# Performance work log

Measured on AMD Instinct MI355X. Metric: run time of the kernel, lower is better.

## Reference

```python
import jax, jax.numpy as jnp
import numpy as np

# dims: L=seq_len, B=batch, D=n_d (hidden), PROJ=n_proj, H=heads, DEPTH=layers, V=vocab
L, B, D, PROJ, H, DEPTH, V = 1024, 4, 1024, 256, 8, 4, 32000
HD = PROJ // H          # head dim = 32
NEG = -10000.0          # additive causal mask value used by Model.set_mask


def setup_inputs() -> dict:
    key = jax.random.key(0)
    ks = jax.random.split(key, 12)
    s = (3.0 / D) ** 0.5  # init used by Model.init_weights (layer_norm-style)
    return {
        "x": jax.random.randint(ks[0], (L, B), 0, V),
        "y": jax.random.randint(ks[1], (L, B), 0, V),
        "hidden": jnp.zeros((DEPTH, B, D), jnp.float32),            # init_hidden
        "emb_W": jax.random.uniform(ks[2], (V, D), jnp.float32, -s, s),
        # SRU++ attention transform per layer: q-proj, kv-proj, output to 3*D (U matrices)
        "W1": jax.random.normal(ks[3], (DEPTH, D, PROJ), jnp.float32) / np.float32(np.sqrt(D)),
        "W2": jax.random.normal(ks[4], (DEPTH, PROJ, 2 * PROJ), jnp.float32) / np.float32(np.sqrt(PROJ)),
        "W3": jax.random.normal(ks[5], (DEPTH, PROJ, 3 * D), jnp.float32) / np.float32(np.sqrt(PROJ)),
        "alpha": jax.random.normal(ks[6], (DEPTH,), jnp.float32) * 0.1,  # rezero scalar (nonzero so attn path is live)
        "weight_c": jax.random.normal(ks[7], (DEPTH, 2 * D), jnp.float32) * 0.1,  # (v_f, v_r)
        # bias = (b_f, b_r); forget bias initialized to highway_bias = -3
        "bias": jnp.concatenate([jnp.full((DEPTH, D), -3.0, jnp.float32), jnp.zeros((DEPTH, D), jnp.float32)], axis=-1),
        "Wout": jax.random.uniform(ks[8], (D, V), jnp.float32, -s, s),
        "bout": jnp.zeros((V,), jnp.float32),
    }


def _attention_transform(h, W1, W2, W3, alpha, mask):
    # SRUppAttention (no memory, no layer_norm, dropout=0)
    z = jnp.einsum('lbd,dp->lbp', h, W1)                 # (L,B,PROJ) query / residual
    kv = jnp.einsum('lbp,pq->lbq', z, W2)                # (L,B,2*PROJ)
    k, v = jnp.split(kv, 2, axis=-1)
    q = z.reshape(L, B, H, HD) * (HD ** -0.5)
    k = k.reshape(L, B, H, HD)
    v = v.reshape(L, B, H, HD)
    scores = jnp.einsum('lbhd,sbhd->bhls', q, k) + mask  # causal additive mask
    attn = jax.nn.softmax(scores, axis=-1)
    out = jnp.einsum('bhls,sbhd->lbhd', attn, v).reshape(L, B, PROJ)
    out = out * alpha + z                                # rezero residual
    return jnp.einsum('lbp,pk->lbk', out, W3)            # U: (L,B,3*D)


def _sru_recurrence(U, residual, c0, vf, vr, bf, br):
    # SRU elementwise highway recurrence (k=3, identity activation, no rescale)
    u = U.reshape(L, B, D, 3)
    u0 = u[..., 0]
    u1 = u[..., 1] + bf
    u2 = u[..., 2] + br

    def step(c, xs):
        u0t, u1t, u2t, rt = xs                           # each (B,D)
        f = jax.nn.sigmoid(u1t + vf * c)
        c = f * c + (1.0 - f) * u0t
        r = jax.nn.sigmoid(u2t + vr * c)
        h = r * c + (1.0 - r) * rt                       # highway on layer input
        return c, h

    c_last, hs = jax.lax.scan(step, c0, (u0, u1, u2, residual))
    return hs, c_last


def reference(x, y, hidden, emb_W, W1, W2, W3, alpha, weight_c, bias, Wout, bout):
    mask = jnp.triu(jnp.full((L, L), NEG, jnp.float32), 1)   # Model.set_mask, mem_len=0
    h = emb_W[x]                                             # (L,B,D) embedding lookup
    for i in range(DEPTH):
        U = _attention_transform(h, W1[i], W2[i], W3[i], alpha[i], mask)
        h, _ = _sru_recurrence(U, h, hidden[i],
                               weight_c[i, :D], weight_c[i, D:],
                               bias[i, :D], bias[i, D:])
    logits = jnp.einsum('lbd,dv->lbv', h, Wout) + bout       # (L,B,V)
    logp = jax.nn.log_softmax(logits, axis=-1)
    loss = -jnp.take_along_axis(logp, y[..., None], axis=-1)[..., 0]  # (L,B) per-token CE
    return loss
```

## Files before the change

### kernel.cpp

```cpp
#include <hip/hip_runtime.h>
#include <hip/hip_bf16.h>
#include <stdint.h>

#define L_ 1024
#define B_ 4
#define D_ 1024
#define PROJ_ 256
#define H_ 8
#define V_ 32000
#define M_ 4096

typedef __bf16 bf16x8 __attribute__((ext_vector_type(8)));
typedef float f32x4 __attribute__((ext_vector_type(4)));

#define AS3(p) ((__attribute__((address_space(3))) void*)(p))
#define AS1(p) ((const __attribute__((address_space(1))) void*)(p))

__global__ __launch_bounds__(256) void k_embed(const int* __restrict__ x,
                                               const float* __restrict__ emb,
                                               __hip_bfloat16* __restrict__ h) {
  int gid = blockIdx.x * 256 + threadIdx.x;
  int row = gid >> 8;
  int d0 = (gid & 255) << 2;
  int tok = x[row];
  const float4 v = *(const float4*)(emb + (size_t)tok * D_ + d0);
  union { __hip_bfloat16 o[4]; uint2 u; } cv;
  cv.o[0] = __float2bfloat16(v.x);
  cv.o[1] = __float2bfloat16(v.y);
  cv.o[2] = __float2bfloat16(v.z);
  cv.o[3] = __float2bfloat16(v.w);
  *(uint2*)(h + (size_t)row * D_ + d0) = cv.u;
}

__global__ __launch_bounds__(256) void k_transpose(const float* __restrict__ in,
                                                   __hip_bfloat16* __restrict__ out,
                                                   int K, int N,
                                                   long in_stride, long out_stride) {
  __shared__ float t[64][65];
  in += (size_t)blockIdx.z * in_stride;
  out += (size_t)blockIdx.z * out_stride;
  int n0 = blockIdx.x * 64, k0 = blockIdx.y * 64;
  int r = threadIdx.x >> 4, c4 = (threadIdx.x & 15) << 2;
#pragma unroll
  for (int p = 0; p < 4; p++) {
    float4 v = *(const float4*)(in + (size_t)(k0 + p * 16 + r) * N + n0 + c4);
    t[p * 16 + r][c4 + 0] = v.x;
    t[p * 16 + r][c4 + 1] = v.y;
    t[p * 16 + r][c4 + 2] = v.z;
    t[p * 16 + r][c4 + 3] = v.w;
  }
  __syncthreads();
  int n = threadIdx.x >> 2, kg = (threadIdx.x & 3) << 4;
  union { __hip_bfloat16 b[16]; uint4 u[2]; } cv;
#pragma unroll
  for (int i = 0; i < 16; i++) cv.b[i] = __float2bfloat16(t[kg + i][n]);
  uint4* op = (uint4*)(out + (size_t)(n0 + n) * K + k0 + kg);
  op[0] = cv.u[0];
  op[1] = cv.u[1];
}

template <bool CLS>
__global__ __launch_bounds__(256) void k_gemm_bt(
    const __hip_bfloat16* __restrict__ A, const __hip_bfloat16* __restrict__ Bt,
    __hip_bfloat16* __restrict__ C, int K, int N,
    const float* __restrict__ bout, const int* __restrict__ y,
    float2* __restrict__ lse, float* __restrict__ logitY) {
  __shared__ __hip_bfloat16 As[128 * 64];
  __shared__ __hip_bfloat16 Bs[128 * 64];
  const int tid = threadIdx.x;
  const int lane = tid & 63, wave = tid >> 6;
  const int quad = lane >> 4, l16 = lane & 15;
  const int wm = wave & 1, wn = wave >> 1;
  const int row0 = blockIdx.x * 128, col0 = blockIdx.y * 128;

  f32x4 acc[4][4] = {};

  const __hip_bfloat16* Abase = A + (size_t)row0 * K;
  const __hip_bfloat16* Bbase = Bt + (size_t)col0 * K;
  const int m_s = tid >> 3;
  const int ko_sw = (((tid & 7) ^ (m_s & 7)) << 3);
  const int xr = l16 & 7;

  for (int k0 = 0; k0 < K; k0 += 64) {
    __syncthreads();
#pragma unroll
    for (int call = 0; call < 4; call++) {
      int m = m_s + call * 32;
      __builtin_amdgcn_global_load_lds(AS1(Abase + (size_t)m * K + k0 + ko_sw),
                                       AS3(As + (call * 256 + wave * 64) * 8),
                                       16, 0, 0);
      __builtin_amdgcn_global_load_lds(AS1(Bbase + (size_t)m * K + k0 + ko_sw),
                                       AS3(Bs + (call * 256 + wave * 64) * 8),
                                       16, 0, 0);
    }
    __syncthreads();
#pragma unroll
    for (int kk = 0; kk < 2; kk++) {
      bf16x8 af[4], bfr[4];
#pragma unroll
      for (int mi = 0; mi < 4; mi++)
        af[mi] = *(const bf16x8*)(As + (wm * 64 + mi * 16 + l16) * 64 +
                                  (((kk * 4 + quad) ^ xr) << 3));
#pragma unroll
      for (int ni = 0; ni < 4; ni++)
        bfr[ni] = *(const bf16x8*)(Bs + (wn * 64 + ni * 16 + l16) * 64 +
                                   (((kk * 4 + quad) ^ xr) << 3));
#pragma unroll
      for (int mi = 0; mi < 4; mi++)
#pragma unroll
        for (int ni = 0; ni < 4; ni++)
          acc[mi][ni] = __builtin_amdgcn_mfma_f32_16x16x32_bf16(af[mi], bfr[ni],
                                                                acc[mi][ni], 0, 0, 0);
    }
  }

  if constexpr (!CLS) {
#pragma unroll
    for (int mi = 0; mi < 4; mi++)
#pragma unroll
      for (int ni = 0; ni < 4; ni++)
#pragma unroll
        for (int r = 0; r < 4; r++) {
          int row = row0 + wm * 64 + mi * 16 + quad * 4 + r;
          int col = col0 + wn * 64 + ni * 16 + l16;
          C[(size_t)row * N + col] = __float2bfloat16(acc[mi][ni][r]);
        }
  } else {
    const int chunk = blockIdx.y * 2 + wn;
    float bv[4];
#pragma unroll
    for (int ni = 0; ni < 4; ni++)
      bv[ni] = bout[col0 + wn * 64 + ni * 16 + l16];
#pragma unroll
    for (int mi = 0; mi < 4; mi++) {
#pragma unroll
      for (int r = 0; r < 4; r++) {
        int row = row0 + wm * 64 + mi * 16 + quad * 4 + r;
        float v0 = acc[mi][0][r] + bv[0];
        float v1 = acc[mi][1][r] + bv[1];
        float v2 = acc[mi][2][r] + bv[2];
        float v3 = acc[mi][3][r] + bv[3];
        int yv = y[row];
        int cb = col0 + wn * 64 + l16;
        if (yv == cb + 0)  logitY[row] = v0;
        if (yv == cb + 16) logitY[row] = v1;
        if (yv == cb + 32) logitY[row] = v2;
        if (yv == cb + 48) logitY[row] = v3;
        float m = fmaxf(fmaxf(v0, v1), fmaxf(v2, v3));
#pragma unroll
        for (int off = 1; off < 16; off <<= 1)
          m = fmaxf(m, __shfl_xor(m, off, 64));
        float s = __expf(v0 - m) + __expf(v1 - m) + __expf(v2 - m) + __expf(v3 - m);
#pragma unroll
        for (int off = 1; off < 16; off <<= 1)
          s += __shfl_xor(s, off, 64);
        if (l16 == 0)
          lse[(size_t)chunk * M_ + row] = make_float2(m, s);
      }
    }
  }
}

__global__ __launch_bounds__(512, 2) void k_gemm_cls256(
    const __hip_bfloat16* __restrict__ A, const __hip_bfloat16* __restrict__ Bt,
    int K, const float* __restrict__ bout, const int* __restrict__ y,
    float2* __restrict__ lse, float* __restrict__ logitY) {
  __shared__ __align__(16) __hip_bfloat16 As[2][16384];
  __shared__ __align__(16) __hip_bfloat16 Bs[2][16384];
  const int tid = threadIdx.x;
  const int lane = tid & 63, wave = tid >> 6;
  const int quad = lane >> 4, l16 = lane & 15;
  const int wm = wave >> 2, wn = wave & 3;

  const int bid = blockIdx.y * 16 + blockIdx.x;
  const int swzb = (bid & 7) * 250 + (bid >> 3);
  const int bx = swzb & 15, by = swzb >> 4;
  const int row0 = bx * 256, col0 = by * 256;

  const int m_l = wave * 8 + (lane >> 3);
  const int sw = ((lane & 7) ^ (lane >> 3)) << 3;
  const __hip_bfloat16* Ag = A + (size_t)(row0 + m_l) * K + sw;
  const __hip_bfloat16* Bg = Bt + (size_t)(col0 + m_l) * K + sw;

#define STAGE_A(buf, r, ko)                                                   \
  __builtin_amdgcn_global_load_lds(AS1(Ag + (size_t)(r) * 64 * K + (ko)),     \
                                   AS3(&As[buf][((r) * 64 + wave * 8) * 64]), \
                                   16, 0, 0)
#define STAGE_B(buf, r, ko)                                                   \
  __builtin_amdgcn_global_load_lds(AS1(Bg + (size_t)(r) * 64 * K + (ko)),     \
                                   AS3(&Bs[buf][((r) * 64 + wave * 8) * 64]), \
                                   16, 0, 0)

  const int aoff = (wm * 128 + l16) * 64;
  const int boff = (wn * 64 + l16) * 64;
  const int cc0 = ((quad) ^ (l16 & 7)) << 3;
  const int cc1 = ((4 + quad) ^ (l16 & 7)) << 3;

  f32x4 acc[8][4] = {};
  bf16x8 a4[4], b4[4];

#define PH_PRE(buf, cck, mlo, READB)                                          \
  do {                                                                        \
    if (READB) {                                                              \
      _Pragma("unroll") for (int ni = 0; ni < 4; ++ni)                        \
          b4[ni] = *(const bf16x8*)(&Bs[buf][boff + ni * 1024 + (cck)]);      \
    }                                                                         \
    _Pragma("unroll") for (int mi = 0; mi < 4; ++mi)                          \
        a4[mi] = *(const bf16x8*)(&As[buf][aoff + ((mlo) + mi) * 1024 + (cck)]); \
  } while (0)

#define PH_MFMA(mlo)                                                          \
  do {                                                                        \
    __builtin_amdgcn_s_barrier();                                             \
    asm volatile("s_waitcnt lgkmcnt(0)" ::: "memory");                        \
    __builtin_amdgcn_sched_barrier(0);                                        \
    __builtin_amdgcn_s_setprio(1);                                            \
    _Pragma("unroll") for (int mi = 0; mi < 4; ++mi)                          \
        _Pragma("unroll") for (int ni = 0; ni < 4; ++ni)                      \
            acc[(mlo) + mi][ni] = __builtin_amdgcn_mfma_f32_16x16x32_bf16(    \
                a4[mi], b4[ni], acc[(mlo) + mi][ni], 0, 0, 0);                \
    __builtin_amdgcn_s_setprio(0);                                            \
  } while (0)

#define BAR() __builtin_amdgcn_s_barrier()

  STAGE_A(0, 0, 0); STAGE_A(0, 1, 0); STAGE_A(0, 2, 0); STAGE_A(0, 3, 0);
  STAGE_B(0, 0, 0); STAGE_B(0, 1, 0); STAGE_B(0, 2, 0); STAGE_B(0, 3, 0);
  STAGE_B(1, 0, 64); STAGE_B(1, 1, 64); STAGE_B(1, 2, 64); STAGE_B(1, 3, 64);
  STAGE_A(1, 0, 64); STAGE_A(1, 2, 64);
  asm volatile("s_waitcnt vmcnt(6)" ::: "memory");
  BAR();

  for (int i = 0; i < 7; ++i) {
    const size_t kT1 = (size_t)i * 128 + 64;
    const size_t kS0 = (size_t)i * 128 + 128;
    const size_t kS1 = (size_t)i * 128 + 192;
    PH_PRE(0, cc0, 0, 1);
    STAGE_A(1, 1, kT1); STAGE_A(1, 3, kT1);
    PH_MFMA(0); BAR();
    PH_PRE(0, cc0, 4, 0);
    PH_MFMA(4); BAR();
    PH_PRE(0, cc1, 0, 1);
    PH_MFMA(0); BAR();
    PH_PRE(0, cc1, 4, 0);
    STAGE_B(0, 0, kS0); STAGE_B(0, 1, kS0);
    PH_MFMA(4);
    asm volatile("s_waitcnt vmcnt(2)" ::: "memory");
    BAR();
    PH_PRE(1, cc0, 0, 1);
    STAGE_B(0, 2, kS0); STAGE_B(0, 3, kS0);
    PH_MFMA(0); BAR();
    PH_PRE(1, cc0, 4, 0);
    STAGE_A(0, 0, kS0); STAGE_A(0, 2, kS0);
    PH_MFMA(4); BAR();
    PH_PRE(1, cc1, 0, 1);
    STAGE_A(0, 1, kS0); STAGE_A(0, 3, kS0);
    PH_MFMA(0); BAR();
    PH_PRE(1, cc1, 4, 0);
    STAGE_B(1, 0, kS1); STAGE_B(1, 1, kS1); STAGE_B(1, 2, kS1); STAGE_B(1, 3, kS1);
    STAGE_A(1, 0, kS1); STAGE_A(1, 2, kS1);
    PH_MFMA(4);
    asm volatile("s_waitcnt vmcnt(6)" ::: "memory");
    BAR();
  }
  {
    const size_t kT1 = (size_t)7 * 128 + 64;
    PH_PRE(0, cc0, 0, 1);
    STAGE_A(1, 1, kT1); STAGE_A(1, 3, kT1);
    PH_MFMA(0); BAR();
    PH_PRE(0, cc0, 4, 0);
    PH_MFMA(4); BAR();
    PH_PRE(0, cc1, 0, 1);
    PH_MFMA(0); BAR();
    PH_PRE(0, cc1, 4, 0);
    PH_MFMA(4);
    asm volatile("s_waitcnt vmcnt(0)" ::: "memory");
    BAR();
    PH_PRE(1, cc0, 0, 1);
    PH_MFMA(0); BAR();
    PH_PRE(1, cc0, 4, 0);
    PH_MFMA(4); BAR();
    PH_PRE(1, cc1, 0, 1);
    PH_MFMA(0); BAR();
    PH_PRE(1, cc1, 4, 0);
    PH_MFMA(4);
  }

  const int chunk = by * 4 + wn;
  float bv[4];
#pragma unroll
  for (int ni = 0; ni < 4; ++ni)
    bv[ni] = bout[col0 + wn * 64 + ni * 16 + l16];
#pragma unroll
  for (int mi = 0; mi < 8; ++mi) {
#pragma unroll
    for (int r = 0; r < 4; ++r) {
      int row = row0 + wm * 128 + mi * 16 + quad * 4 + r;
      float v0 = acc[mi][0][r] + bv[0];
      float v1 = acc[mi][1][r] + bv[1];
      float v2 = acc[mi][2][r] + bv[2];
      float v3 = acc[mi][3][r] + bv[3];
      int yv = y[row];
      int cb = col0 + wn * 64 + l16;
      if (yv == cb + 0)  logitY[row] = v0;
      if (yv == cb + 16) logitY[row] = v1;
      if (yv == cb + 32) logitY[row] = v2;
      if (yv == cb + 48) logitY[row] = v3;
      float m = fmaxf(fmaxf(v0, v1), fmaxf(v2, v3));
#pragma unroll
      for (int off = 1; off < 16; off <<= 1)
        m = fmaxf(m, __shfl_xor(m, off, 64));
      float s = __expf(v0 - m) + __expf(v1 - m) + __expf(v2 - m) + __expf(v3 - m);
#pragma unroll
      for (int off = 1; off < 16; off <<= 1)
        s += __shfl_xor(s, off, 64);
      if (l16 == 0)
        lse[(size_t)chunk * M_ + row] = make_float2(m, s);
    }
  }
#undef STAGE_A
#undef STAGE_B
#undef PH_PRE
#undef PH_MFMA
#undef BAR
}

__global__ __launch_bounds__(256) void k_gemm_cls_f32(
    const __hip_bfloat16* __restrict__ A, const float* __restrict__ B,
    int K, int N, const float* __restrict__ bout, const int* __restrict__ y,
    float2* __restrict__ lse, float* __restrict__ logitY) {
  __shared__ __hip_bfloat16 As[128 * 40];
  __shared__ __hip_bfloat16 Bs[128 * 40];
  const int tid = threadIdx.x;
  const int lane = tid & 63, wave = tid >> 6;
  const int quad = lane >> 4, l16 = lane & 15;
  const int wm = wave & 1, wn = wave >> 1;
  const int row0 = blockIdx.x * 128, col0 = blockIdx.y * 128;
  f32x4 acc[4][4] = {};
  const int a_m = tid >> 1, a_k = (tid & 1) << 4;
  const int b_k = tid >> 3, b_n = (tid & 7) << 4;
  for (int k0 = 0; k0 < K; k0 += 32) {
    const uint4* ap = (const uint4*)(A + (size_t)(row0 + a_m) * K + k0 + a_k);
    uint4 av0 = ap[0];
    uint4 av1 = ap[1];
    const float* bp = B + (size_t)(k0 + b_k) * N + col0 + b_n;
    float4 bv0 = *(const float4*)(bp + 0);
    float4 bv1 = *(const float4*)(bp + 4);
    float4 bv2 = *(const float4*)(bp + 8);
    float4 bv3 = *(const float4*)(bp + 12);
    __syncthreads();
    *(uint4*)(As + a_m * 40 + a_k) = av0;
    *(uint4*)(As + a_m * 40 + a_k + 8) = av1;
    {
      float tmp[16] = {bv0.x, bv0.y, bv0.z, bv0.w, bv1.x, bv1.y, bv1.z, bv1.w,
                       bv2.x, bv2.y, bv2.z, bv2.w, bv3.x, bv3.y, bv3.z, bv3.w};
#pragma unroll
      for (int j = 0; j < 16; j++)
        Bs[(b_n + j) * 40 + b_k] = __float2bfloat16(tmp[j]);
    }
    __syncthreads();
    bf16x8 af[4], bfr[4];
#pragma unroll
    for (int mi = 0; mi < 4; mi++)
      af[mi] = *(const bf16x8*)(As + (wm * 64 + mi * 16 + l16) * 40 + quad * 8);
#pragma unroll
    for (int ni = 0; ni < 4; ni++)
      bfr[ni] = *(const bf16x8*)(Bs + (wn * 64 + ni * 16 + l16) * 40 + quad * 8);
#pragma unroll
    for (int mi = 0; mi < 4; mi++)
#pragma unroll
      for (int ni = 0; ni < 4; ni++)
        acc[mi][ni] = __builtin_amdgcn_mfma_f32_16x16x32_bf16(af[mi], bfr[ni],
                                                              acc[mi][ni], 0, 0, 0);
  }
  const int chunk = blockIdx.y * 2 + wn;
  float bv[4];
#pragma unroll
  for (int ni = 0; ni < 4; ni++)
    bv[ni] = bout[col0 + wn * 64 + ni * 16 + l16];
#pragma unroll
  for (int mi = 0; mi < 4; mi++) {
#pragma unroll
    for (int r = 0; r < 4; r++) {
      int row = row0 + wm * 64 + mi * 16 + quad * 4 + r;
      float v0 = acc[mi][0][r] + bv[0];
      float v1 = acc[mi][1][r] + bv[1];
      float v2 = acc[mi][2][r] + bv[2];
      float v3 = acc[mi][3][r] + bv[3];
      int yv = y[row];
      int cb = col0 + wn * 64 + l16;
      if (yv == cb + 0)  logitY[row] = v0;
      if (yv == cb + 16) logitY[row] = v1;
      if (yv == cb + 32) logitY[row] = v2;
      if (yv == cb + 48) logitY[row] = v3;
      float m = fmaxf(fmaxf(v0, v1), fmaxf(v2, v3));
#pragma unroll
      for (int off = 1; off < 16; off <<= 1)
        m = fmaxf(m, __shfl_xor(m, off, 64));
      float s = __expf(v0 - m) + __expf(v1 - m) + __expf(v2 - m) + __expf(v3 - m);
#pragma unroll
      for (int off = 1; off < 16; off <<= 1)
        s += __shfl_xor(s, off, 64);
      if (l16 == 0)
        lse[(size_t)chunk * M_ + row] = make_float2(m, s);
    }
  }
}

__global__ __launch_bounds__(256) void k_attn_mfma(
    const __hip_bfloat16* __restrict__ z, const __hip_bfloat16* __restrict__ kv,
    __hip_bfloat16* __restrict__ ao, const float* __restrict__ alpha_p) {
  __shared__ __hip_bfloat16 Qs[64 * 40];
  __shared__ __hip_bfloat16 Ks[128 * 40];
  __shared__ __hip_bfloat16 Vt[32 * 136];
  __shared__ __hip_bfloat16 Ps[64 * 136];
  const int tid = threadIdx.x;
  const int lane = tid & 63, wave = tid >> 6;
  const int quad = lane >> 4, l16 = lane & 15;
  const int bh = blockIdx.y, b = bh >> 3, h = bh & 7;
  const int q0 = blockIdx.x * 64;
  const float scale = 0.17677669529663687f;

  {
    int r = tid >> 2, c = (tid & 3) << 3;
    *(uint4*)(Qs + r * 40 + c) =
        *(const uint4*)(z + ((size_t)(q0 + r) * B_ + b) * PROJ_ + h * 32 + c);
  }

  float m_i[4] = {-1e30f, -1e30f, -1e30f, -1e30f};
  float l_i[4] = {0.f, 0.f, 0.f, 0.f};
  f32x4 o_acc[2] = {};

  const int ntile = (q0 + 191) >> 7;

  for (int t = 0; t < ntile; t++) {
    const int s0 = t << 7;
    __syncthreads();
    {
      int r = tid >> 1, c = (tid & 1) << 4;
      const uint4* kp =
          (const uint4*)(kv + ((size_t)(s0 + r) * B_ + b) * 512 + h * 32 + c);
      *(uint4*)(Ks + r * 40 + c) = kp[0];
      *(uint4*)(Ks + r * 40 + c + 8) = kp[1];
    }
    {
      int s = tid >> 1, dbase = (tid & 1) << 4;
      const __hip_bfloat16* vp =
          kv + ((size_t)(s0 + s) * B_ + b) * 512 + 256 + h * 32 + dbase;
      union { uint4 u; __hip_bfloat16 e[8]; } t0, t1;
      t0.u = *(const uint4*)vp;
      t1.u = *(const uint4*)(vp + 8);
#pragma unroll
      for (int j = 0; j < 8; j++) {
        Vt[(dbase + j) * 136 + s] = t0.e[j];
        Vt[(dbase + 8 + j) * 136 + s] = t1.e[j];
      }
    }
    __syncthreads();

    f32x4 sacc[8] = {};
    {
      bf16x8 aq = *(const bf16x8*)(Qs + (wave * 16 + l16) * 40 + quad * 8);
#pragma unroll
      for (int ni = 0; ni < 8; ni++) {
        bf16x8 bk = *(const bf16x8*)(Ks + (ni * 16 + l16) * 40 + quad * 8);
        sacc[ni] = __builtin_amdgcn_mfma_f32_16x16x32_bf16(aq, bk, sacc[ni], 0, 0, 0);
      }
    }

#pragma unroll
    for (int r = 0; r < 4; r++) {
      const int qrow = q0 + wave * 16 + quad * 4 + r;
      float mx = -1e30f;
#pragma unroll
      for (int ni = 0; ni < 8; ni++) {
        int s = s0 + ni * 16 + l16;
        float v = (s <= qrow) ? sacc[ni][r] * scale : -1e30f;
        sacc[ni][r] = v;
        mx = fmaxf(mx, v);
      }
#pragma unroll
      for (int off = 1; off < 16; off <<= 1)
        mx = fmaxf(mx, __shfl_xor(mx, off, 64));
      float mnew = fmaxf(m_i[r], mx);
      float al = __expf(m_i[r] - mnew);
      m_i[r] = mnew;
      float ps = 0.f;
#pragma unroll
      for (int ni = 0; ni < 8; ni++) {
        float p = __expf(sacc[ni][r] - mnew);
        Ps[(wave * 16 + quad * 4 + r) * 136 + ni * 16 + l16] = __float2bfloat16(p);
        ps += p;
      }
#pragma unroll
      for (int off = 1; off < 16; off <<= 1)
        ps += __shfl_xor(ps, off, 64);
      l_i[r] = l_i[r] * al + ps;
      o_acc[0][r] *= al;
      o_acc[1][r] *= al;
    }

#pragma unroll
    for (int ks = 0; ks < 4; ks++) {
      bf16x8 ap = *(const bf16x8*)(Ps + (wave * 16 + l16) * 136 + ks * 32 + quad * 8);
#pragma unroll
      for (int ni = 0; ni < 2; ni++) {
        bf16x8 bv = *(const bf16x8*)(Vt + (ni * 16 + l16) * 136 + ks * 32 + quad * 8);
        o_acc[ni] = __builtin_amdgcn_mfma_f32_16x16x32_bf16(ap, bv, o_acc[ni], 0, 0, 0);
      }
    }
  }

  const float arz = alpha_p[0];
#pragma unroll
  for (int ni = 0; ni < 2; ni++)
#pragma unroll
    for (int r = 0; r < 4; r++) {
      int row = q0 + wave * 16 + quad * 4 + r;
      size_t oi = ((size_t)row * B_ + b) * PROJ_ + h * 32 + ni * 16 + l16;
      float res = __bfloat162float(z[oi]);
      ao[oi] = __float2bfloat16(o_acc[ni][r] / l_i[r] * arz + res);
    }
}

__global__ __launch_bounds__(64) void k_sru(const __hip_bfloat16* __restrict__ U,
                                            __hip_bfloat16* __restrict__ h,
                                            const float* __restrict__ hidden,
                                            const float* __restrict__ wc,
                                            const float* __restrict__ bias) {
  int tid = blockIdx.x * 64 + threadIdx.x;
  int b = tid >> 10, d = tid & 1023;
  float vf = wc[d], vr = wc[D_ + d];
  float bfs = bias[d], brs = bias[D_ + d];
  float c = hidden[b * D_ + d];
  const __hip_bfloat16* up = U + (size_t)b * 3 * D_ + 3 * d;
  __hip_bfloat16* hp = h + (size_t)b * D_ + d;
  const int US = B_ * 3 * D_, HS = B_ * D_;
  for (int l0 = 0; l0 < L_; l0 += 8) {
    float u0[8], u1[8], u2[8], rs[8];
#pragma unroll
    for (int j = 0; j < 8; j++) {
      u0[j] = __bfloat162float(up[(size_t)j * US + 0]);
      u1[j] = __bfloat162float(up[(size_t)j * US + 1]);
      u2[j] = __bfloat162float(up[(size_t)j * US + 2]);
      rs[j] = __bfloat162float(hp[(size_t)j * HS]);
    }
#pragma unroll
    for (int j = 0; j < 8; j++) {
      float f = __builtin_amdgcn_rcpf(1.f + __expf(-(u1[j] + bfs + vf * c)));
      c = u0[j] + f * (c - u0[j]);
      float r = __builtin_amdgcn_rcpf(1.f + __expf(-(u2[j] + brs + vr * c)));
      hp[(size_t)j * HS] = __float2bfloat16(rs[j] + r * (c - rs[j]));
    }
    up += (size_t)8 * US;
    hp += (size_t)8 * HS;
  }
}

__global__ __launch_bounds__(256) void k_finalize(const float2* __restrict__ lse,
                                                  const float* __restrict__ logitY,
                                                  float* __restrict__ out) {
  int row = blockIdx.x * 256 + threadIdx.x;
  float M = -1e30f, S = 0.f;
  for (int c = 0; c < V_ / 64; c++) {
    float2 p = lse[(size_t)c * M_ + row];
    if (p.x > M) {
      S = S * __expf(M - p.x) + p.y;
      M = p.x;
    } else {
      S += p.y * __expf(p.x - M);
    }
  }
  out[row] = M + logf(S) - logitY[row];
}

extern "C" void kernel_launch(void* const* d_in, const int* in_sizes, int n_in,
                              void* d_out, int out_size, void* d_ws, size_t ws_size,
                              hipStream_t stream) {
  const int* x = (const int*)d_in[0];
  const int* y = (const int*)d_in[1];
  const float* hidden = (const float*)d_in[2];
  const float* emb = (const float*)d_in[3];
  const float* W1 = (const float*)d_in[4];
  const float* W2 = (const float*)d_in[5];
  const float* W3 = (const float*)d_in[6];
  const float* alpha = (const float*)d_in[7];
  const float* wc = (const float*)d_in[8];
  const float* bias = (const float*)d_in[9];
  const float* Wout = (const float*)d_in[10];
  const float* bout = (const float*)d_in[11];

  char* ws = (char*)d_ws;
  __hip_bfloat16* h16  = (__hip_bfloat16*)(ws + 0);
  __hip_bfloat16* z16  = (__hip_bfloat16*)(ws + 8388608);
  __hip_bfloat16* kv16 = (__hip_bfloat16*)(ws + 10485760);
  __hip_bfloat16* ao16 = (__hip_bfloat16*)(ws + 14680064);
  __hip_bfloat16* W1t  = (__hip_bfloat16*)(ws + 16777216);
  __hip_bfloat16* W2t  = (__hip_bfloat16*)(ws + 18874368);
  __hip_bfloat16* W3t  = (__hip_bfloat16*)(ws + 19922944);
  __hip_bfloat16* U16  = (__hip_bfloat16*)(ws + 26214400);
  const bool fast = ws_size >= 109723648ull;
  __hip_bfloat16* Woutt = (__hip_bfloat16*)(ws + 26214400);
  float2* lse    = (float2*)(ws + (fast ? 93323264u : 26214400u));
  float* logitY  = (float*)(ws + (fast ? 109707264u : 42598400u));
  float* out     = (float*)d_out;

  k_embed<<<4096, 256, 0, stream>>>(x, emb, h16);
  k_transpose<<<dim3(4, 16, 4), 256, 0, stream>>>(W1, W1t, D_, PROJ_,
                                                  (long)D_ * PROJ_, (long)PROJ_ * D_);
  k_transpose<<<dim3(8, 4, 4), 256, 0, stream>>>(W2, W2t, PROJ_, 2 * PROJ_,
                                                 (long)PROJ_ * 2 * PROJ_,
                                                 (long)2 * PROJ_ * PROJ_);
  k_transpose<<<dim3(48, 4, 4), 256, 0, stream>>>(W3, W3t, PROJ_, 3 * D_,
                                                  (long)PROJ_ * 3 * D_,
                                                  (long)3 * D_ * PROJ_);
  for (int i = 0; i < 4; i++) {
    k_gemm_bt<false><<<dim3(32, 2), 256, 0, stream>>>(
        h16, W1t + (size_t)i * PROJ_ * D_, z16, D_, PROJ_,
        nullptr, nullptr, nullptr, nullptr);
    k_gemm_bt<false><<<dim3(32, 4), 256, 0, stream>>>(
        z16, W2t + (size_t)i * 2 * PROJ_ * PROJ_, kv16, PROJ_, 2 * PROJ_,
        nullptr, nullptr, nullptr, nullptr);
    k_attn_mfma<<<dim3(16, 32), 256, 0, stream>>>(z16, kv16, ao16, alpha + i);
    k_gemm_bt<false><<<dim3(32, 24), 256, 0, stream>>>(
        ao16, W3t + (size_t)i * 3 * D_ * PROJ_, U16, PROJ_, 3 * D_,
        nullptr, nullptr, nullptr, nullptr);
    k_sru<<<64, 64, 0, stream>>>(U16, h16, hidden + (size_t)i * B_ * D_,
                                 wc + (size_t)i * 2 * D_, bias + (size_t)i * 2 * D_);
  }
  if (fast) {
    k_transpose<<<dim3(500, 16, 1), 256, 0, stream>>>(Wout, Woutt, D_, V_, 0, 0);
    k_gemm_cls256<<<dim3(16, 125), 512, 0, stream>>>(h16, Woutt, D_, bout, y,
                                                     lse, logitY);
  } else {
    k_gemm_cls_f32<<<dim3(32, V_ / 128), 256, 0, stream>>>(
        h16, Wout, D_, V_, bout, y, lse, logitY);
  }
  k_finalize<<<16, 256, 0, stream>>>(lse, logitY, out);
}
```

Baseline: 1.442 ms.

## Reorder classifier GEMM phases to keep two B fragments resident and restage loads

Reorganizes the inner schedule of the vocab-projection GEMM so that both k-halves of the B fragment are held in separate registers (b0, b1), and the A fragment quadrants are iterated with B reused rather than re-read from LDS. The global-to-LDS staging of A and B is reshuffled so all four A rows of the next half-tile load together and B loads are spread across later phases, with vmcnt waits adjusted accordingly. The intent is fewer LDS reads of B and a more balanced overlap of global loads with MFMA work. It costs extra VGPRs for the second B fragment, and the changed wait counts could expose load latency or race if miscounted.

```diff
diff --git a/kernel.cpp b/kernel.cpp
--- a/kernel.cpp
+++ b/kernel.cpp
@@ -197,19 +197,21 @@
   const int cc1 = ((4 + quad) ^ (l16 & 7)) << 3;
 
   f32x4 acc[8][4] = {};
-  bf16x8 a4[4], b4[4];
-
-#define PH_PRE(buf, cck, mlo, READB)                                          \
+  bf16x8 a4[4], b0[4], b1[4];
+
+#define DS_B(buf, breg, cck)                                                  \
   do {                                                                        \
-    if (READB) {                                                              \
-      _Pragma("unroll") for (int ni = 0; ni < 4; ++ni)                        \
-          b4[ni] = *(const bf16x8*)(&Bs[buf][boff + ni * 1024 + (cck)]);      \
-    }                                                                         \
+    _Pragma("unroll") for (int ni = 0; ni < 4; ++ni)                          \
+        breg[ni] = *(const bf16x8*)(&Bs[buf][boff + ni * 1024 + (cck)]);      \
+  } while (0)
+
+#define DS_A(buf, mlo, cck)                                                   \
+  do {                                                                        \
     _Pragma("unroll") for (int mi = 0; mi < 4; ++mi)                          \
         a4[mi] = *(const bf16x8*)(&As[buf][aoff + ((mlo) + mi) * 1024 + (cck)]); \
   } while (0)
 
-#define PH_MFMA(mlo)                                                          \
+#define MFMA_Q(mlo, breg)                                                     \
   do {                                                                        \
     __builtin_amdgcn_s_barrier();                                             \
     asm volatile("s_waitcnt lgkmcnt(0)" ::: "memory");                        \
@@ -218,7 +220,7 @@
     _Pragma("unroll") for (int mi = 0; mi < 4; ++mi)                          \
         _Pragma("unroll") for (int ni = 0; ni < 4; ++ni)                      \
             acc[(mlo) + mi][ni] = __builtin_amdgcn_mfma_f32_16x16x32_bf16(    \
-                a4[mi], b4[ni], acc[(mlo) + mi][ni], 0, 0, 0);                \
+                a4[mi], breg[ni], acc[(mlo) + mi][ni], 0, 0, 0);              \
     __builtin_amdgcn_s_setprio(0);                                            \
   } while (0)
 
@@ -227,63 +229,61 @@
   STAGE_A(0, 0, 0); STAGE_A(0, 1, 0); STAGE_A(0, 2, 0); STAGE_A(0, 3, 0);
   STAGE_B(0, 0, 0); STAGE_B(0, 1, 0); STAGE_B(0, 2, 0); STAGE_B(0, 3, 0);
   STAGE_B(1, 0, 64); STAGE_B(1, 1, 64); STAGE_B(1, 2, 64); STAGE_B(1, 3, 64);
-  STAGE_A(1, 0, 64); STAGE_A(1, 2, 64);
-  asm volatile("s_waitcnt vmcnt(6)" ::: "memory");
+  asm volatile("s_waitcnt vmcnt(4)" ::: "memory");
   BAR();
 
   for (int i = 0; i < 7; ++i) {
     const size_t kT1 = (size_t)i * 128 + 64;
-    const size_t kS0 = (size_t)i * 128 + 128;
-    const size_t kS1 = (size_t)i * 128 + 192;
-    PH_PRE(0, cc0, 0, 1);
-    STAGE_A(1, 1, kT1); STAGE_A(1, 3, kT1);
-    PH_MFMA(0); BAR();
-    PH_PRE(0, cc0, 4, 0);
-    PH_MFMA(4); BAR();
-    PH_PRE(0, cc1, 0, 1);
-    PH_MFMA(0); BAR();
-    PH_PRE(0, cc1, 4, 0);
-    STAGE_B(0, 0, kS0); STAGE_B(0, 1, kS0);
-    PH_MFMA(4);
-    asm volatile("s_waitcnt vmcnt(2)" ::: "memory");
+    const size_t kN0 = (size_t)i * 128 + 128;
+    const size_t kN1 = (size_t)i * 128 + 192;
+    DS_B(0, b0, cc0); DS_A(0, 0, cc0);
+    STAGE_A(1, 0, kT1); STAGE_A(1, 1, kT1); STAGE_A(1, 2, kT1); STAGE_A(1, 3, kT1);
+    MFMA_Q(0, b0); BAR();
+    DS_B(0, b1, cc1); DS_A(0, 0, cc1);
+    MFMA_Q(0, b1); BAR();
+    DS_A(0, 4, cc0);
+    STAGE_B(0, 0, kN0); STAGE_B(0, 1, kN0);
+    MFMA_Q(4, b0); BAR();
+    DS_A(0, 4, cc1);
+    STAGE_B(0, 2, kN0); STAGE_B(0, 3, kN0);
+    MFMA_Q(4, b1);
+    asm volatile("s_waitcnt vmcnt(4)" ::: "memory");
     BAR();
-    PH_PRE(1, cc0, 0, 1);
-    STAGE_B(0, 2, kS0); STAGE_B(0, 3, kS0);
-    PH_MFMA(0); BAR();
-    PH_PRE(1, cc0, 4, 0);
-    STAGE_A(0, 0, kS0); STAGE_A(0, 2, kS0);
-    PH_MFMA(4); BAR();
-    PH_PRE(1, cc1, 0, 1);
-    STAGE_A(0, 1, kS0); STAGE_A(0, 3, kS0);
-    PH_MFMA(0); BAR();
-    PH_PRE(1, cc1, 4, 0);
-    STAGE_B(1, 0, kS1); STAGE_B(1, 1, kS1); STAGE_B(1, 2, kS1); STAGE_B(1, 3, kS1);
-    STAGE_A(1, 0, kS1); STAGE_A(1, 2, kS1);
-    PH_MFMA(4);
-    asm volatile("s_waitcnt vmcnt(6)" ::: "memory");
+    DS_B(1, b0, cc0); DS_A(1, 0, cc0);
+    STAGE_A(0, 0, kN0); STAGE_A(0, 1, kN0); STAGE_A(0, 2, kN0); STAGE_A(0, 3, kN0);
+    MFMA_Q(0, b0); BAR();
+    DS_B(1, b1, cc1); DS_A(1, 0, cc1);
+    MFMA_Q(0, b1); BAR();
+    DS_A(1, 4, cc0);
+    STAGE_B(1, 0, kN1); STAGE_B(1, 1, kN1);
+    MFMA_Q(4, b0); BAR();
+    DS_A(1, 4, cc1);
+    STAGE_B(1, 2, kN1); STAGE_B(1, 3, kN1);
+    MFMA_Q(4, b1);
+    asm volatile("s_waitcnt vmcnt(4)" ::: "memory");
     BAR();
   }
   {
     const size_t kT1 = (size_t)7 * 128 + 64;
-    PH_PRE(0, cc0, 0, 1);
-    STAGE_A(1, 1, kT1); STAGE_A(1, 3, kT1);
-    PH_MFMA(0); BAR();
-    PH_PRE(0, cc0, 4, 0);
-    PH_MFMA(4); BAR();
-    PH_PRE(0, cc1, 0, 1);
-    PH_MFMA(0); BAR();
-    PH_PRE(0, cc1, 4, 0);
-    PH_MFMA(4);
+    DS_B(0, b0, cc0); DS_A(0, 0, cc0);
+    STAGE_A(1, 0, kT1); STAGE_A(1, 1, kT1); STAGE_A(1, 2, kT1); STAGE_A(1, 3, kT1);
+    MFMA_Q(0, b0); BAR();
+    DS_B(0, b1, cc1); DS_A(0, 0, cc1);
+    MFMA_Q(0, b1); BAR();
+    DS_A(0, 4, cc0);
+    MFMA_Q(4, b0); BAR();
+    DS_A(0, 4, cc1);
+    MFMA_Q(4, b1);
     asm volatile("s_waitcnt vmcnt(0)" ::: "memory");
     BAR();
-    PH_PRE(1, cc0, 0, 1);
-    PH_MFMA(0); BAR();
-    PH_PRE(1, cc0, 4, 0);
-    PH_MFMA(4); BAR();
-    PH_PRE(1, cc1, 0, 1);
-    PH_MFMA(0); BAR();
-    PH_PRE(1, cc1, 4, 0);
-    PH_MFMA(4);
+    DS_B(1, b0, cc0); DS_A(1, 0, cc0);
+    MFMA_Q(0, b0); BAR();
+    DS_B(1, b1, cc1); DS_A(1, 0, cc1);
+    MFMA_Q(0, b1); BAR();
+    DS_A(1, 4, cc0);
+    MFMA_Q(4, b0); BAR();
+    DS_A(1, 4, cc1);
+    MFMA_Q(4, b1);
   }
 
   const int chunk = by * 4 + wn;
@@ -320,8 +320,9 @@
   }
 #undef STAGE_A
 #undef STAGE_B
-#undef PH_PRE
-#undef PH_MFMA
+#undef DS_A
+#undef DS_B
+#undef MFMA_Q
 #undef BAR
 }
 
```

After: 1.444 ms. About the same (+0.1%).
